# Performance work log

Hardware: AMD Instinct MI355X
Metric: run time of the kernel (lower is better)

The kernel has to match this reference:

```python
import jax, jax.numpy as jnp
import numpy as np

B, S, D, C = 16, 1024, 768, 2


def setup_inputs() -> dict:
    key = jax.random.key(0)
    ks = jax.random.split(key, 6)
    sc = 1.0 / np.sqrt(D)
    return {
        "tokens": jax.random.normal(ks[0], (B, S, D), jnp.float32),
        "Wk": jax.random.normal(ks[1], (D, D), jnp.float32) * sc,
        "bk": jnp.zeros((D,), jnp.float32),
        "Wq": jax.random.normal(ks[2], (D, D), jnp.float32) * sc,
        "bq": jnp.zeros((D,), jnp.float32),
        "Wv": jax.random.normal(ks[3], (D, D), jnp.float32) * sc,
        "bv": jnp.zeros((D,), jnp.float32),
        "ln_g": jnp.ones((S, D), jnp.float32),
        "ln_b": jnp.zeros((S, D), jnp.float32),
        "W_sgsa": jax.random.normal(ks[4], (D, 1), jnp.float32) * sc,
        "b_sgsa": jnp.zeros((1,), jnp.float32),
        "W_fnn": jax.random.normal(ks[5], (4 * D, C), jnp.float32) * (1.0 / np.sqrt(4 * D)),
        "b_fnn": jnp.zeros((C,), jnp.float32),
    }


def reference(tokens, Wk, bk, Wq, bq, Wv, bv, ln_g, ln_b, W_sgsa, b_sgsa, W_fnn, b_fnn):
    fact = 1.0 / jnp.sqrt(jnp.asarray(D, tokens.dtype))
    # --- token-wise single-head attention ---
    K = tokens @ Wk + bk                                  # [B,S,D]
    Q = tokens @ Wq + bq
    V = tokens @ Wv + bv
    att = jax.nn.softmax(jnp.einsum('bsd,btd->bst', Q, K) * fact, axis=-1)  # [B,S,S]
    out = jnp.einsum('bst,btd->bsd', att, V)              # [B,S,D]
    # --- LayerNorm over last two dims (S,D) jointly, eps=1e-8 ---
    mu = jnp.mean(out, axis=(1, 2), keepdims=True)
    var = jnp.var(out, axis=(1, 2), keepdims=True)
    out_ln = (out - mu) / jnp.sqrt(var + 1e-8) * ln_g + ln_b
    # --- feature-wise attention (same K/Q/V weights, transposed bmm) ---
    K_N = out_ln @ Wk + bk
    Q_N = out_ln @ Wq + bq
    V_N = out_ln @ Wv + bv
    att_N = jax.nn.softmax(jnp.einsum('bsd,bse->bde', Q_N, K_N) * fact, axis=-1)  # [B,D,D]
    out_N = jnp.einsum('bsd,bde->bse', V_N, att_N)        # [B,S,D]
    # --- SGSA gating ---
    gate = out_N @ W_sgsa + b_sgsa                        # [B,S,1]
    out_sgsa = gate * out_N                               # [B,S,D]
    # --- concat, dual pooling, FC ---
    cat = jnp.concatenate([tokens, out_sgsa], axis=2)     # [B,S,2D]
    pooled = jnp.concatenate([jnp.mean(cat, axis=1), jnp.max(cat, axis=1)], axis=1)  # [B,4D]
    return pooled @ W_fnn + b_fnn                         # [B,C]
```

## Files before the change

### kernel.cpp

```cpp
#include <hip/hip_runtime.h>

#define BB 16
#define SS 1024
#define DD 768

typedef _Float16 f16x4 __attribute__((ext_vector_type(4)));
typedef _Float16 f16x8 __attribute__((ext_vector_type(8)));
typedef float f32x4 __attribute__((ext_vector_type(4)));

__device__ __forceinline__ void gload_lds16(const void* g, void* l) {
  __builtin_amdgcn_global_load_lds(
      (const __attribute__((address_space(1))) unsigned int*)g,
      (__attribute__((address_space(3))) unsigned int*)l, 16, 0, 0);
}

template<int OUTM, int BIAS>
__global__ __launch_bounds__(512, 4) void gemm256(
    const _Float16* __restrict__ A, long long aB,
    const _Float16* __restrict__ Bt, long long bB,
    const float* __restrict__ bias, int biasB,
    void* __restrict__ Cv, long long cB,
    float* __restrict__ aux,
    int M, int N, int K)
{
  __shared__ __attribute__((aligned(16))) _Float16 lds[24576];
  const int t = threadIdx.x;
  int z, m0, n0;
  if (OUTM == 3 || OUTM == 4) {
    const int lin = blockIdx.x + 18 * blockIdx.y;
    const int xcd = lin & 7, idx = lin >> 3;
    const int mt  = xcd * 8 + idx / 18;
    const int zn  = idx % 18;
    z  = zn / 6;
    n0 = (zn % 6) * 128;
    m0 = mt * 256;
  } else {
    z = blockIdx.z;
    m0 = blockIdx.x * 256;
    n0 = blockIdx.y * 128;
  }
  const _Float16* Ab = A + (size_t)z * aB;
  const _Float16* Bb = Bt + (size_t)z * bB;

  const int l = t & 63, w = t >> 6;
  const int wr = (w >> 1) * 64, wc = (w & 1) * 64;
  const int lrow = l & 15, kq = l >> 4;
  const int qread = ((lrow & 1) << 2) | (kq ^ ((lrow >> 1) & 3));
  const int fragoff = (lrow >> 1) * 128 + qread * 16;

  const int sp = t >> 3, sq = t & 7;
  const int srow = 2 * sp + (sq >> 2);
  const int schk = (sq & 3) ^ (sp & 3);
  const size_t ldK = (size_t)K * 2;
  const char* pA0 = (const char*)Ab + (size_t)(m0 + srow) * ldK + schk * 16;
  const char* pA1 = pA0 + (size_t)128 * ldK;
  const char* pB0 = (const char*)Bb + (size_t)(n0 + srow) * ldK + schk * 16;
  char* const ldsb = (char*)lds;
  const int dstt = t * 16;

  auto stg = [&](int T, int sd) {
    const char* ga0 = pA0 + (size_t)T * 64;
    const char* ga1 = pA1 + (size_t)T * 64;
    const char* gb  = pB0 + (size_t)T * 64;
    char* d = ldsb + sd * 24576 + dstt;
    gload_lds16(ga0, d);
    gload_lds16(ga1, d + 8192);
    gload_lds16(gb,  d + 16384);
  };

  f32x4 acc[4][4] = {};
  f16x8 af[4], bf[4];

  stg(0, 0);

  const int NT = K >> 5;
  for (int T = 0; T < NT; ++T) {
    const int sd = T & 1, sn = sd ^ 1;
    const char* Abase = ldsb + sd * 24576;
    const char* Bbase = Abase + 16384;

    asm volatile("s_waitcnt vmcnt(0)" ::: "memory");
    __builtin_amdgcn_s_barrier();
    asm volatile("" ::: "memory");
    if (T + 1 < NT) stg(T + 1, sn);

    #pragma unroll
    for (int n = 0; n < 4; n++)
      bf[n] = *(const f16x8*)(Bbase + (wc + n * 16) * 64 + fragoff);
    #pragma unroll
    for (int mi = 0; mi < 4; mi++)
      af[mi] = *(const f16x8*)(Abase + (wr + mi * 16) * 64 + fragoff);

    __builtin_amdgcn_s_setprio(1);
    #pragma unroll
    for (int mi = 0; mi < 4; mi++)
      #pragma unroll
      for (int n = 0; n < 4; n++)
        acc[mi][n] = __builtin_amdgcn_mfma_f32_16x16x32_f16(af[mi], bf[n], acc[mi][n], 0, 0, 0);
    __builtin_amdgcn_s_setprio(0);
  }

  const int crow = (l >> 4) * 4, ccol = l & 15;
  #pragma unroll
  for (int m = 0; m < 4; ++m) {
    const int rq = m0 + wr + m * 16 + crow;
    #pragma unroll
    for (int n = 0; n < 4; ++n) {
      const int c = n0 + wc + n * 16 + ccol;
      const float bv = BIAS ? bias[(size_t)z * biasB + c] : 0.0f;
      if (OUTM == 0) {
        float* C = (float*)Cv + (size_t)z * cB;
        #pragma unroll
        for (int j = 0; j < 4; j++)
          C[(size_t)(rq + j) * N + c] = acc[m][n][j] + bv;
      } else if (OUTM == 5 || OUTM == 6) {
        _Float16* C = (_Float16*)Cv + (size_t)z * cB;
        #pragma unroll
        for (int j = 0; j < 4; j++)
          C[(size_t)(rq + j) * N + c] = (_Float16)(acc[m][n][j] + bv);
      } else {
        _Float16* C = (_Float16*)Cv + (size_t)z * cB;
        const bool tr = (OUTM == 3) ? (z == 2) : (z < 2);
        if (tr) {
          const int bq = rq >> 10, s = rq & 1023;
          f16x4 o;
          #pragma unroll
          for (int j = 0; j < 4; j++) o[j] = (_Float16)(acc[m][n][j] + bv);
          *(f16x4*)&C[((size_t)(bq * N + c) << 10) + s] = o;
        } else {
          #pragma unroll
          for (int j = 0; j < 4; j++)
            C[(size_t)(rq + j) * N + c] = (_Float16)(acc[m][n][j] + bv);
        }
      }
    }
  }

  if (OUTM == 6) {
    float ls = 0.0f, lq = 0.0f;
    #pragma unroll
    for (int m = 0; m < 4; ++m)
      #pragma unroll
      for (int n = 0; n < 4; ++n)
        #pragma unroll
        for (int j = 0; j < 4; j++) {
          const float v = acc[m][n][j];
          ls += v; lq += v * v;
        }
    __syncthreads();
    float* red = (float*)lds;
    red[t] = ls; red[512 + t] = lq;
    __syncthreads();
    #pragma unroll
    for (int off = 256; off > 0; off >>= 1) {
      if (t < off) { red[t] += red[t + off]; red[512 + t] += red[512 + t + off]; }
      __syncthreads();
    }
    if (t == 0) {
      const int chunk = blockIdx.x * 6 + blockIdx.y;
      aux[(z * 24 + chunk) * 2]     = red[0];
      aux[(z * 24 + chunk) * 2 + 1] = red[512];
    }
  }
}

__global__ __launch_bounds__(256) void cast_pool(const float* __restrict__ tokens,
                                                 _Float16* __restrict__ tok_h,
                                                 float* __restrict__ tpart)
{
  const int b = blockIdx.y, ch = blockIdx.x, t = threadIdx.x;
  float s0 = 0, s1 = 0, s2 = 0;
  float x0 = -3.4e38f, x1 = -3.4e38f, x2 = -3.4e38f;
  const size_t rowbase = ((size_t)b * SS + ch * 32) * DD;
  for (int i = 0; i < 32; i++) {
    const float* tr = tokens + rowbase + (size_t)i * DD;
    _Float16* hw = tok_h + rowbase + (size_t)i * DD;
    float t0 = tr[t], t1 = tr[t + 256], t2 = tr[t + 512];
    hw[t] = (_Float16)t0; hw[t + 256] = (_Float16)t1; hw[t + 512] = (_Float16)t2;
    s0 += t0; s1 += t1; s2 += t2;
    x0 = fmaxf(x0, t0); x1 = fmaxf(x1, t1); x2 = fmaxf(x2, t2);
  }
  float* pb = tpart + (size_t)(b * 32 + ch) * 1536;
  pb[t] = s0;        pb[t + 256] = s1;        pb[t + 512] = s2;
  pb[768 + t] = x0;  pb[768 + t + 256] = x1;  pb[768 + t + 512] = x2;
}

__global__ __launch_bounds__(256) void transpose_f2h(const float* __restrict__ in,
                                                     _Float16* __restrict__ outp, int R, int C)
{
  __shared__ float tile[32][33];
  const int r0 = blockIdx.y * 32, c0 = blockIdx.x * 32;
  const int tx = threadIdx.x & 31, ty = threadIdx.x >> 5;
  #pragma unroll
  for (int i = 0; i < 4; i++)
    tile[ty + i * 8][tx] = in[(size_t)(r0 + ty + i * 8) * C + c0 + tx];
  __syncthreads();
  #pragma unroll
  for (int i = 0; i < 4; i++)
    outp[(size_t)(c0 + ty + i * 8) * R + r0 + tx] = (_Float16)tile[tx][ty + i * 8];
}

__global__ __launch_bounds__(256) void transpose_b2h(const _Float16* __restrict__ in, long long inB,
                                                     _Float16* __restrict__ outp, long long outB,
                                                     int R, int C)
{
  __shared__ _Float16 tile[32][33];
  const _Float16* ib = in + (size_t)blockIdx.z * inB;
  _Float16* ob = outp + (size_t)blockIdx.z * outB;
  const int r0 = blockIdx.y * 32, c0 = blockIdx.x * 32;
  const int tx = threadIdx.x & 31, ty = threadIdx.x >> 5;
  #pragma unroll
  for (int i = 0; i < 4; i++)
    tile[ty + i * 8][tx] = ib[(size_t)(r0 + ty + i * 8) * C + c0 + tx];
  __syncthreads();
  #pragma unroll
  for (int i = 0; i < 4; i++)
    ob[(size_t)(c0 + ty + i * 8) * R + r0 + tx] = tile[tx][ty + i * 8];
}

__global__ void pack_bias(const float* __restrict__ a, const float* __restrict__ b,
                          const float* __restrict__ c, float* __restrict__ o)
{
  int t = blockIdx.x * 256 + threadIdx.x;
  if (t < 768) o[t] = a[t];
  else if (t < 1536) o[t] = b[t - 768];
  else if (t < 2304) o[t] = c[t - 1536];
}

template<int VPT>
__global__ __launch_bounds__(256) void softmax_h2h(const _Float16* __restrict__ X,
                                                   _Float16* __restrict__ Y,
                                                   int L, float scale)
{
  const size_t base = (size_t)blockIdx.x * L;
  const int t = threadIdx.x;
  float v[VPT];
  float m = -3.4e38f;
  #pragma unroll
  for (int j = 0; j < VPT; j++) { v[j] = (float)X[base + t + j * 256]; m = fmaxf(m, v[j]); }
  __shared__ float red[256];
  red[t] = m; __syncthreads();
  #pragma unroll
  for (int off = 128; off > 0; off >>= 1) {
    if (t < off) red[t] = fmaxf(red[t], red[t + off]);
    __syncthreads();
  }
  m = red[0]; __syncthreads();
  float s = 0.0f;
  #pragma unroll
  for (int j = 0; j < VPT; j++) { v[j] = __expf((v[j] - m) * scale); s += v[j]; }
  red[t] = s; __syncthreads();
  #pragma unroll
  for (int off = 128; off > 0; off >>= 1) {
    if (t < off) red[t] += red[t + off];
    __syncthreads();
  }
  const float inv = 1.0f / red[0];
  #pragma unroll
  for (int j = 0; j < VPT; j++) Y[base + t + j * 256] = (_Float16)(v[j] * inv);
}

__global__ void ln_final(const float* __restrict__ part, float* __restrict__ stats)
{
  const int b = blockIdx.x, t = threadIdx.x;
  float s = 0.0f, q = 0.0f;
  if (t < 24) { s = part[(b * 24 + t) * 2]; q = part[(b * 24 + t) * 2 + 1]; }
  #pragma unroll
  for (int off = 32; off > 0; off >>= 1) { s += __shfl_down(s, off); q += __shfl_down(q, off); }
  if (t == 0) {
    const float invN = 1.0f / (float)(SS * DD);
    float mu = s * invN;
    float var = q * invN - mu * mu;
    stats[b * 2] = mu;
    stats[b * 2 + 1] = rsqrtf(var + 1e-8f);
  }
}

__global__ __launch_bounds__(256) void ln_apply_h(_Float16* __restrict__ data,
                                                  const float* __restrict__ g,
                                                  const float* __restrict__ bta,
                                                  const float* __restrict__ stats)
{
  const long long n4 = (long long)BB * SS * DD / 4;
  const int SD4 = SS * DD / 4;
  for (long long i = (long long)blockIdx.x * 256 + threadIdx.x; i < n4;
       i += (long long)gridDim.x * 256) {
    const int b = (int)(i / SD4);
    const int sd4 = (int)(i - (long long)b * SD4);
    const float mu = stats[b * 2], rs = stats[b * 2 + 1];
    f16x4 v = ((const f16x4*)data)[i];
    float4 gg = ((const float4*)g)[sd4];
    float4 bb = ((const float4*)bta)[sd4];
    f16x4 r;
    r[0] = (_Float16)(((float)v[0] - mu) * rs * gg.x + bb.x);
    r[1] = (_Float16)(((float)v[1] - mu) * rs * gg.y + bb.y);
    r[2] = (_Float16)(((float)v[2] - mu) * rs * gg.z + bb.z);
    r[3] = (_Float16)(((float)v[3] - mu) * rs * gg.w + bb.w);
    ((f16x4*)data)[i] = r;
  }
}

__global__ __launch_bounds__(256) void gate_k(const _Float16* __restrict__ outN,
                                              const float* __restrict__ wsg,
                                              const float* __restrict__ bsg,
                                              float* __restrict__ gate)
{
  const int row = blockIdx.x * 4 + (threadIdx.x >> 6);
  const int l = threadIdx.x & 63;
  const _Float16* src = outN + (size_t)row * DD;
  float s = 0.0f;
  #pragma unroll
  for (int i = 0; i < 12; i++) s += (float)src[l + i * 64] * wsg[l + i * 64];
  #pragma unroll
  for (int off = 32; off > 0; off >>= 1) s += __shfl_down(s, off);
  if (l == 0) gate[row] = s + bsg[0];
}

__global__ __launch_bounds__(256) void opool(const _Float16* __restrict__ outN,
                                             const float* __restrict__ gate,
                                             float* __restrict__ opart)
{
  const int b = blockIdx.y, ch = blockIdx.x, t = threadIdx.x;
  float s0 = 0, s1 = 0, s2 = 0;
  float x0 = -3.4e38f, x1 = -3.4e38f, x2 = -3.4e38f;
  const size_t rowbase = ((size_t)b * SS + ch * 32) * DD;
  for (int i = 0; i < 32; i++) {
    const _Float16* orw = outN + rowbase + (size_t)i * DD;
    const float g = gate[b * SS + ch * 32 + i];
    float o0 = (float)orw[t] * g, o1 = (float)orw[t + 256] * g, o2 = (float)orw[t + 512] * g;
    s0 += o0; s1 += o1; s2 += o2;
    x0 = fmaxf(x0, o0); x1 = fmaxf(x1, o1); x2 = fmaxf(x2, o2);
  }
  float* pb = opart + (size_t)(b * 32 + ch) * 1536;
  pb[t] = s0;        pb[t + 256] = s1;        pb[t + 512] = s2;
  pb[768 + t] = x0;  pb[768 + t + 256] = x1;  pb[768 + t + 512] = x2;
}

__global__ __launch_bounds__(256) void pool_final(const float* __restrict__ tpart,
                                                  const float* __restrict__ opart,
                                                  float* __restrict__ pooled)
{
  const int idx = blockIdx.x * 256 + threadIdx.x;
  const int b = idx / DD, d = idx - b * DD;
  float st = 0, so = 0, xt = -3.4e38f, xo = -3.4e38f;
  for (int ch = 0; ch < 32; ch++) {
    const float* tb = tpart + (size_t)(b * 32 + ch) * 1536;
    const float* ob = opart + (size_t)(b * 32 + ch) * 1536;
    st += tb[d]; xt = fmaxf(xt, tb[768 + d]);
    so += ob[d]; xo = fmaxf(xo, ob[768 + d]);
  }
  const float inv = 1.0f / (float)SS;
  pooled[(size_t)b * 3072 + d]        = st * inv;
  pooled[(size_t)b * 3072 + 768 + d]  = so * inv;
  pooled[(size_t)b * 3072 + 1536 + d] = xt;
  pooled[(size_t)b * 3072 + 2304 + d] = xo;
}

__global__ __launch_bounds__(256) void fc_k(const float* __restrict__ pooled,
                                            const float* __restrict__ Wf,
                                            const float* __restrict__ bf,
                                            float* __restrict__ outp)
{
  const int b = blockIdx.x, t = threadIdx.x;
  float p0 = 0.0f, p1 = 0.0f;
  #pragma unroll
  for (int i = 0; i < 12; i++) {
    const int j = t + i * 256;
    const float pv = pooled[(size_t)b * 3072 + j];
    p0 += pv * Wf[j * 2];
    p1 += pv * Wf[j * 2 + 1];
  }
  __shared__ float r0[256], r1[256];
  r0[t] = p0; r1[t] = p1; __syncthreads();
  #pragma unroll
  for (int off = 128; off > 0; off >>= 1) {
    if (t < off) { r0[t] += r0[t + off]; r1[t] += r1[t + off]; }
    __syncthreads();
  }
  if (t == 0) {
    outp[b * 2 + 0] = r0[0] + bf[0];
    outp[b * 2 + 1] = r1[0] + bf[1];
  }
}

extern "C" void kernel_launch(void* const* d_in, const int* in_sizes, int n_in,
                              void* d_out, int out_size, void* d_ws, size_t ws_size,
                              hipStream_t stream)
{
  const float* tokens = (const float*)d_in[0];
  const float* Wk  = (const float*)d_in[1];
  const float* bk  = (const float*)d_in[2];
  const float* Wq  = (const float*)d_in[3];
  const float* bq  = (const float*)d_in[4];
  const float* Wv  = (const float*)d_in[5];
  const float* bv  = (const float*)d_in[6];
  const float* lng = (const float*)d_in[7];
  const float* lnb = (const float*)d_in[8];
  const float* Wsg = (const float*)d_in[9];
  const float* bsg = (const float*)d_in[10];
  const float* Wf  = (const float*)d_in[11];
  const float* bfn = (const float*)d_in[12];
  float* outp = (float*)d_out;
  (void)in_sizes; (void)n_in; (void)out_size; (void)ws_size;

  char* ws = (char*)d_ws;
  _Float16* R0   = (_Float16*)(ws + 0);
  _Float16* R1   = (_Float16*)(ws + 67108864);
  _Float16* R2   = (_Float16*)(ws + 92274688);
  _Float16* R3   = (_Float16*)(ws + 117440512);
  _Float16* R4   = (_Float16*)(ws + 142606336);
  _Float16* R5   = (_Float16*)(ws + 167772160);
  _Float16* Wt   = (_Float16*)(ws + 201326592);
  float* bias3   = (float*)(ws + 204865536);
  float* lnpart  = (float*)(ws + 204874752);
  float* stats   = (float*)(ws + 204878848);
  float* gate    = (float*)(ws + 204878976);
  float* tpart   = (float*)(ws + 204944512);
  float* opart   = (float*)(ws + 208090240);
  float* pooled  = (float*)(ws + 211235968);

  const float fact = 0.036084391824351615f;
  const long long SD = (long long)SS * DD;
  const long long S2 = (long long)SS * SS;
  const long long D2 = (long long)DD * DD;
  const long long PL = (long long)BB * SD;

  cast_pool<<<dim3(32, BB), 256, 0, stream>>>(tokens, R1, tpart);
  transpose_f2h<<<dim3(24, 24), 256, 0, stream>>>(Wk, Wt,               768, 768);
  transpose_f2h<<<dim3(24, 24), 256, 0, stream>>>(Wq, Wt + 589824,      768, 768);
  transpose_f2h<<<dim3(24, 24), 256, 0, stream>>>(Wv, Wt + 2 * 589824,  768, 768);
  pack_bias<<<9, 256, 0, stream>>>(bk, bq, bv, bias3);

  gemm256<3, 1><<<dim3(18, 64), 512, 0, stream>>>(R1, 0, Wt, 589824, bias3, 768,
                                                  (void*)R2, PL, nullptr, BB * SS, DD, DD);
  gemm256<5, 0><<<dim3(4, 8, 16), 512, 0, stream>>>(R3, SD, R2, SD, nullptr, 0,
                                                    (void*)R0, S2, nullptr, SS, SS, DD);
  softmax_h2h<4><<<BB * SS, 256, 0, stream>>>(R0, R5, SS, fact);
  gemm256<6, 0><<<dim3(4, 6, 16), 512, 0, stream>>>(R5, S2, R4, SD, nullptr, 0,
                                                    (void*)R1, SD, lnpart, SS, DD, SS);
  ln_final<<<16, 64, 0, stream>>>(lnpart, stats);
  ln_apply_h<<<2048, 256, 0, stream>>>(R1, lng, lnb, stats);

  gemm256<4, 1><<<dim3(18, 64), 512, 0, stream>>>(R1, 0, Wt, 589824, bias3, 768,
                                                  (void*)R2, PL, nullptr, BB * SS, DD, DD);
  gemm256<5, 0><<<dim3(3, 6, 16), 512, 0, stream>>>(R3, SD, R2, SD, nullptr, 0,
                                                    (void*)R0, D2, nullptr, DD, DD, SS);
  softmax_h2h<3><<<BB * DD, 256, 0, stream>>>(R0, R5, DD, fact);
  transpose_b2h<<<dim3(24, 24, 16), 256, 0, stream>>>(R5, D2, R1, D2, DD, DD);
  gemm256<5, 0><<<dim3(4, 6, 16), 512, 0, stream>>>(R4, SD, R1, D2, nullptr, 0,
                                                    (void*)R5, SD, nullptr, SS, DD, DD);

  gate_k<<<4096, 256, 0, stream>>>(R5, Wsg, bsg, gate);
  opool<<<dim3(32, BB), 256, 0, stream>>>(R5, gate, opart);
  pool_final<<<48, 256, 0, stream>>>(tpart, opart, pooled);
  fc_k<<<16, 256, 0, stream>>>(pooled, Wf, bfn, outp);
}
```

Measured before the change: 413.6 us.

## Fold Wq·Wkᵀ into one matrix for token attention and triple-buffer GEMM LDS

Measured after the change: 419.6 us. About the same (+1.5%).

```diff
diff --git a/kernel.cpp b/kernel.cpp
--- a/kernel.cpp
+++ b/kernel.cpp
@@ -23,7 +23,7 @@
     float* __restrict__ aux,
     int M, int N, int K)
 {
-  __shared__ __attribute__((aligned(16))) _Float16 lds[24576];
+  __shared__ __attribute__((aligned(16))) _Float16 lds[36864];
   const int t = threadIdx.x;
   int z, m0, n0;
   if (OUTM == 3 || OUTM == 4) {
@@ -58,11 +58,11 @@
   char* const ldsb = (char*)lds;
   const int dstt = t * 16;
 
-  auto stg = [&](int T, int sd) {
+  auto stg = [&](int T, int sl) {
     const char* ga0 = pA0 + (size_t)T * 64;
     const char* ga1 = pA1 + (size_t)T * 64;
     const char* gb  = pB0 + (size_t)T * 64;
-    char* d = ldsb + sd * 24576 + dstt;
+    char* d = ldsb + sl * 24576 + dstt;
     gload_lds16(ga0, d);
     gload_lds16(ga1, d + 8192);
     gload_lds16(gb,  d + 16384);
@@ -72,17 +72,19 @@
   f16x8 af[4], bf[4];
 
   stg(0, 0);
+  stg(1, 1);
 
   const int NT = K >> 5;
+  int sl = 0, slw = 2;
   for (int T = 0; T < NT; ++T) {
-    const int sd = T & 1, sn = sd ^ 1;
-    const char* Abase = ldsb + sd * 24576;
+    const char* Abase = ldsb + sl * 24576;
     const char* Bbase = Abase + 16384;
 
-    asm volatile("s_waitcnt vmcnt(0)" ::: "memory");
+    if (T == NT - 1) asm volatile("s_waitcnt vmcnt(0)" ::: "memory");
+    else             asm volatile("s_waitcnt vmcnt(3)" ::: "memory");
     __builtin_amdgcn_s_barrier();
     asm volatile("" ::: "memory");
-    if (T + 1 < NT) stg(T + 1, sn);
+    if (T + 2 < NT) stg(T + 2, slw);
 
     #pragma unroll
     for (int n = 0; n < 4; n++)
@@ -98,6 +100,9 @@
       for (int n = 0; n < 4; n++)
         acc[mi][n] = __builtin_amdgcn_mfma_f32_16x16x32_f16(af[mi], bf[n], acc[mi][n], 0, 0, 0);
     __builtin_amdgcn_s_setprio(0);
+
+    sl = (sl == 2) ? 0 : sl + 1;
+    slw = (slw == 2) ? 0 : slw + 1;
   }
 
   const int crow = (l >> 4) * 4, ccol = l & 15;
@@ -120,7 +125,7 @@
           C[(size_t)(rq + j) * N + c] = (_Float16)(acc[m][n][j] + bv);
       } else {
         _Float16* C = (_Float16*)Cv + (size_t)z * cB;
-        const bool tr = (OUTM == 3) ? (z == 2) : (z < 2);
+        const bool tr = (OUTM == 2) ? true : ((OUTM == 3) ? (z == 2) : (z < 2));
         if (tr) {
           const int bq = rq >> 10, s = rq & 1023;
           f16x4 o;
@@ -185,6 +190,18 @@
   pb[768 + t] = x0;  pb[768 + t + 256] = x1;  pb[768 + t + 512] = x2;
 }
 
+__global__ __launch_bounds__(256) void cast_f2h(const float* __restrict__ in,
+                                                _Float16* __restrict__ outp, long long n4)
+{
+  for (long long i = (long long)blockIdx.x * 256 + threadIdx.x; i < n4;
+       i += (long long)gridDim.x * 256) {
+    float4 v = ((const float4*)in)[i];
+    f16x4 r;
+    r[0] = (_Float16)v.x; r[1] = (_Float16)v.y; r[2] = (_Float16)v.z; r[3] = (_Float16)v.w;
+    ((f16x4*)outp)[i] = r;
+  }
+}
+
 __global__ __launch_bounds__(256) void transpose_f2h(const float* __restrict__ in,
                                                      _Float16* __restrict__ outp, int R, int C)
 {
@@ -227,17 +244,38 @@
   else if (t < 2304) o[t] = c[t - 1536];
 }
 
-template<int VPT>
+__global__ __launch_bounds__(256) void mv_k(const float* __restrict__ W,
+                                            const float* __restrict__ v,
+                                            float* __restrict__ w2)
+{
+  const int row = blockIdx.x * 4 + (threadIdx.x >> 6);
+  const int l = threadIdx.x & 63;
+  const float* src = W + (size_t)row * DD;
+  float s = 0.0f;
+  #pragma unroll
+  for (int i = 0; i < 12; i++) s += src[l + i * 64] * v[l + i * 64];
+  #pragma unroll
+  for (int off = 32; off > 0; off >>= 1) s += __shfl_down(s, off);
+  if (l == 0) w2[row] = s;
+}
+
+template<int VPT, int BIASV>
 __global__ __launch_bounds__(256) void softmax_h2h(const _Float16* __restrict__ X,
                                                    _Float16* __restrict__ Y,
+                                                   const float* __restrict__ v2,
                                                    int L, float scale)
 {
   const size_t base = (size_t)blockIdx.x * L;
   const int t = threadIdx.x;
+  const float* vb = BIASV ? (v2 + (((size_t)blockIdx.x >> 10) << 10)) : nullptr;
   float v[VPT];
   float m = -3.4e38f;
   #pragma unroll
-  for (int j = 0; j < VPT; j++) { v[j] = (float)X[base + t + j * 256]; m = fmaxf(m, v[j]); }
+  for (int j = 0; j < VPT; j++) {
+    v[j] = (float)X[base + t + j * 256];
+    if (BIASV) v[j] += vb[t + j * 256];
+    m = fmaxf(m, v[j]);
+  }
   __shared__ float red[256];
   red[t] = m; __syncthreads();
   #pragma unroll
@@ -300,20 +338,20 @@
   }
 }
 
-__global__ __launch_bounds__(256) void gate_k(const _Float16* __restrict__ outN,
-                                              const float* __restrict__ wsg,
-                                              const float* __restrict__ bsg,
-                                              float* __restrict__ gate)
+__global__ __launch_bounds__(256) void gate_k(const _Float16* __restrict__ src,
+                                              const float* __restrict__ wv,
+                                              const float* __restrict__ b0,
+                                              float* __restrict__ outv)
 {
   const int row = blockIdx.x * 4 + (threadIdx.x >> 6);
   const int l = threadIdx.x & 63;
-  const _Float16* src = outN + (size_t)row * DD;
+  const _Float16* s0 = src + (size_t)row * DD;
   float s = 0.0f;
   #pragma unroll
-  for (int i = 0; i < 12; i++) s += (float)src[l + i * 64] * wsg[l + i * 64];
+  for (int i = 0; i < 12; i++) s += (float)s0[l + i * 64] * wv[l + i * 64];
   #pragma unroll
   for (int off = 32; off > 0; off >>= 1) s += __shfl_down(s, off);
-  if (l == 0) gate[row] = s + bsg[0];
+  if (l == 0) outv[row] = s + b0[0];
 }
 
 __global__ __launch_bounds__(256) void opool(const _Float16* __restrict__ outN,
@@ -418,6 +456,13 @@
   float* tpart   = (float*)(ws + 204944512);
   float* opart   = (float*)(ws + 208090240);
   float* pooled  = (float*)(ws + 211235968);
+  float* v2      = (float*)(ws + 211432576);
+  float* w2      = (float*)(ws + 211498112);
+  float* fzero   = (float*)(ws + 211501184);
+
+  _Float16* Wq_h = R2;
+  _Float16* Wk_h = R2 + 589824;
+  _Float16* Mt   = R2 + 2 * 589824;
 
   const float fact = 0.036084391824351615f;
   const long long SD = (long long)SS * DD;
@@ -425,17 +470,28 @@
   const long long D2 = (long long)DD * DD;
   const long long PL = (long long)BB * SD;
 
+  hipMemsetAsync((void*)fzero, 0, 4, stream);
+
   cast_pool<<<dim3(32, BB), 256, 0, stream>>>(tokens, R1, tpart);
   transpose_f2h<<<dim3(24, 24), 256, 0, stream>>>(Wk, Wt,               768, 768);
   transpose_f2h<<<dim3(24, 24), 256, 0, stream>>>(Wq, Wt + 589824,      768, 768);
   transpose_f2h<<<dim3(24, 24), 256, 0, stream>>>(Wv, Wt + 2 * 589824,  768, 768);
+  cast_f2h<<<576, 256, 0, stream>>>(Wq, Wq_h, 147456);
+  cast_f2h<<<576, 256, 0, stream>>>(Wk, Wk_h, 147456);
   pack_bias<<<9, 256, 0, stream>>>(bk, bq, bv, bias3);
-
-  gemm256<3, 1><<<dim3(18, 64), 512, 0, stream>>>(R1, 0, Wt, 589824, bias3, 768,
-                                                  (void*)R2, PL, nullptr, BB * SS, DD, DD);
-  gemm256<5, 0><<<dim3(4, 8, 16), 512, 0, stream>>>(R3, SD, R2, SD, nullptr, 0,
+  mv_k<<<192, 256, 0, stream>>>(Wk, bq, w2);
+
+  gemm256<5, 0><<<dim3(3, 6, 1), 512, 0, stream>>>(Wk_h, 0, Wq_h, 0, nullptr, 0,
+                                                   (void*)Mt, 0, nullptr, DD, DD, DD);
+  gemm256<2, 1><<<dim3(64, 6, 1), 512, 0, stream>>>(R1, 0, Wt + 2 * 589824, 0, bv, 0,
+                                                    (void*)R4, 0, nullptr, BB * SS, DD, DD);
+  gemm256<5, 0><<<dim3(64, 6, 1), 512, 0, stream>>>(R1, 0, Mt, 0, nullptr, 0,
+                                                    (void*)R3, 0, nullptr, BB * SS, DD, DD);
+  gate_k<<<4096, 256, 0, stream>>>(R1, w2, fzero, v2);
+
+  gemm256<5, 0><<<dim3(4, 8, 16), 512, 0, stream>>>(R3, SD, R1, SD, nullptr, 0,
                                                     (void*)R0, S2, nullptr, SS, SS, DD);
-  softmax_h2h<4><<<BB * SS, 256, 0, stream>>>(R0, R5, SS, fact);
+  softmax_h2h<4, 1><<<BB * SS, 256, 0, stream>>>(R0, R5, v2, SS, fact);
   gemm256<6, 0><<<dim3(4, 6, 16), 512, 0, stream>>>(R5, S2, R4, SD, nullptr, 0,
                                                     (void*)R1, SD, lnpart, SS, DD, SS);
   ln_final<<<16, 64, 0, stream>>>(lnpart, stats);
@@ -445,7 +501,7 @@
                                                   (void*)R2, PL, nullptr, BB * SS, DD, DD);
   gemm256<5, 0><<<dim3(3, 6, 16), 512, 0, stream>>>(R3, SD, R2, SD, nullptr, 0,
                                                     (void*)R0, D2, nullptr, DD, DD, SS);
-  softmax_h2h<3><<<BB * DD, 256, 0, stream>>>(R0, R5, DD, fact);
+  softmax_h2h<3, 0><<<BB * DD, 256, 0, stream>>>(R0, R5, nullptr, DD, fact);
   transpose_b2h<<<dim3(24, 24, 16), 256, 0, stream>>>(R5, D2, R1, D2, DD, DD);
   gemm256<5, 0><<<dim3(4, 6, 16), 512, 0, stream>>>(R4, SD, R1, D2, nullptr, 0,
                                                     (void*)R5, SD, nullptr, SS, DD, DD);
```
